# Kernel optimization log

Hardware: AMD Instinct MI355X
Metric: run time of the kernel (lower is better)

Reference implementation:

```python
import jax, jax.numpy as jnp
import numpy as np

BITS = 4
MAXQ = (1 << BITS) - 1  # 15
GROUPSIZE = 128
IN_F = 8192
OUT_F = 8192
PACK = 32 // BITS  # 8 values per int32


def setup_inputs() -> dict:
    key = jax.random.key(0)
    k_x, k_w, k_z, k_s, k_b = jax.random.split(key, 5)
    groups = IN_F // GROUPSIZE
    x = jax.random.normal(k_x, (4, 32, IN_F), dtype=jnp.float32)
    # bit-packed int32 weight / zeros (random bit patterns are valid quantized data)
    qweight = jax.random.randint(k_w, (IN_F // PACK, OUT_F), 0, 2**31 - 1, dtype=jnp.int32)
    qzeros = jax.random.randint(k_z, (groups, OUT_F // PACK), 0, 2**31 - 1, dtype=jnp.int32)
    scales = (jax.random.uniform(k_s, (groups, OUT_F), dtype=jnp.float32) * 0.01 + 1e-3)
    g_idx = (jnp.arange(IN_F, dtype=jnp.int32) // GROUPSIZE).astype(jnp.int32)
    bias = jax.random.normal(k_b, (OUT_F,), dtype=jnp.float32) * 0.01
    return {"x": x, "qweight": qweight, "qzeros": qzeros, "scales": scales,
            "g_idx": g_idx, "bias": bias}


def _dequant(qweight, qzeros, scales, g_idx):
    shifts = jnp.arange(0, 32, BITS, dtype=jnp.int32)  # [PACK]
    # unpack weights along the input dim: [in/PACK, PACK, out] -> [in, out]
    w = (qweight[:, None, :] >> shifts[None, :, None]) & MAXQ
    w = w.reshape(-1, qweight.shape[1])
    # unpack zeros along the output dim: [groups, out/PACK, PACK] -> [groups, out]
    # GPTQ stores (zero - 1), so add 1 back
    z = ((qzeros[:, :, None] >> shifts[None, None, :]) & MAXQ) + 1
    z = z.reshape(qzeros.shape[0], -1)
    # per-group dequant: W[i, o] = scales[g_idx[i], o] * (w[i, o] - z[g_idx[i], o])
    W = scales[g_idx] * (w.astype(scales.dtype) - z[g_idx].astype(scales.dtype))
    return W  # [in, out]


def reference(x, qweight, qzeros, scales, g_idx, bias):
    W = _dequant(qweight, qzeros, scales, g_idx)
    out = jnp.einsum('bsi,io->bso', x, W) + bias
    return out
```

## Files before the change

### kernel.cpp

```cpp
#include <hip/hip_runtime.h>
#include <hip/hip_bf16.h>
#include <stdint.h>


#define IN_F 8192
#define OUT_F 8192
#define MROWS 128
#define KSPLIT 8
#define KCHUNK 1024
#define BM 64

typedef short short8_t __attribute__((ext_vector_type(8)));
typedef float float4_t __attribute__((ext_vector_type(4)));
typedef float float16_t __attribute__((ext_vector_type(16)));

__global__ void reduce_out(const unsigned short* __restrict__ part,
                           const float* __restrict__ bias,
                           float* __restrict__ out) {
  const int i = (blockIdx.x * 256 + threadIdx.x) * 4;
  const int o = i & (OUT_F - 1);
  float4_t s = *(const float4_t*)(bias + o);
#pragma unroll
  for (int sl = 0; sl < KSPLIT; ++sl) {
    union { ushort2 u2[2]; unsigned short us[4]; } p;
    *(uint2*)&p = *(const uint2*)(part + (size_t)sl * MROWS * OUT_F + i);
    s.x += __uint_as_float((unsigned)p.us[0] << 16);
    s.y += __uint_as_float((unsigned)p.us[1] << 16);
    s.z += __uint_as_float((unsigned)p.us[2] << 16);
    s.w += __uint_as_float((unsigned)p.us[3] << 16);
  }
  *(float4_t*)(out + i) = s;
}

__global__ __launch_bounds__(1024, 4) void gptq_gemm(
    const float* __restrict__ x,
    const int* __restrict__ qweight,
    const int* __restrict__ qzeros,
    const float* __restrict__ scales,
    unsigned short* __restrict__ part)
{
  __shared__ unsigned short As[BM * KCHUNK];

  const int tid  = threadIdx.x;
  const int lane = tid & 63;
  const int l31  = lane & 31;
  const int half = lane >> 5;
  const int wv   = tid >> 6;

  const int bid = blockIdx.x;
  const int kb  = bid >> 5;
  const int mb  = (bid >> 4) & 1;
  const int nb  = bid & 15;

  const int kc0 = kb * KCHUNK;
  const int m0  = mb * BM;
  const int g0  = kc0 >> 7;
  const int kp_base = (kc0 >> 3) + half;
  const int goff = (wv & 3) * 2;

  const int col = nb * 512 + wv * 32 + l31;

  int   qw[3][8];
  float sc[3];
  int   zq[3];

  auto prefetch = [&](int i, int buf) {
    const int ge = (i + goff) & 7;
    const int kp = kp_base + ge * 16;
#pragma unroll
    for (int ks = 0; ks < 8; ++ks)
      qw[buf][ks] = qweight[(size_t)(kp + ks * 2) * OUT_F + col];
    const int gg_abs = g0 + ge;
    sc[buf] = scales[gg_abs * OUT_F + col];
    zq[buf] = qzeros[gg_abs * (OUT_F / 8) + (col >> 3)];
  };

  prefetch(0, 0);
  prefetch(1, 1);

  for (int rq = 0; rq < 4; ++rq) {
    const int rl = wv * 4 + rq;
    const float* grow = x + (size_t)(m0 + rl) * IN_F + kc0;
#pragma unroll
    for (int hf = 0; hf < 2; ++hf) {
      const int p = hf * 64 + lane;
      const int c = (p & 0x70) | ((p ^ (rl & 15)) & 15);
      float4_t a = *(const float4_t*)(grow + c * 8);
      float4_t b = *(const float4_t*)(grow + c * 8 + 4);
      union { short8_t v; __hip_bfloat162 h[4]; } u;
      u.h[0] = __float22bfloat162_rn(make_float2(a.x, a.y));
      u.h[1] = __float22bfloat162_rn(make_float2(a.z, a.w));
      u.h[2] = __float22bfloat162_rn(make_float2(b.x, b.y));
      u.h[3] = __float22bfloat162_rn(make_float2(b.z, b.w));
      *(short8_t*)(As + ((size_t)rl * 128 + p) * 8) = u.v;
    }
  }
  __syncthreads();

  float16_t acc[2];
#pragma unroll
  for (int mt = 0; mt < 2; ++mt)
#pragma unroll
    for (int r = 0; r < 16; ++r) acc[mt][r] = 0.f;

#pragma unroll
  for (int g = 0; g < 8; ++g) {
    const int cur = g % 3;
    const int ge  = (g + goff) & 7;

    if (g + 2 < 8) prefetch(g + 2, (g + 2) % 3);

    const int z = ((zq[cur] >> (4 * (col & 7))) & 15) + 1;
    const float zb = -sc[cur] * (float)z;
    const float s = sc[cur];

#pragma unroll
    for (int ks = 0; ks < 8; ++ks) {
      const int c = ge * 16 + ks * 2 + half;
      const int p = (c & 0x70) | ((c ^ (l31 & 15)) & 15);

      short8_t af[2];
#pragma unroll
      for (int mt = 0; mt < 2; ++mt)
        af[mt] = *(const short8_t*)(As + ((size_t)(mt * 32 + l31) * 128 + p) * 8);

      union { short8_t v; unsigned u[4]; } bw;
      const unsigned q  = (unsigned)qw[cur][ks];
      const unsigned qe = q & 0x0F0F0F0Fu;
      const unsigned qo = (q >> 4) & 0x0F0F0F0Fu;
#pragma unroll
      for (int jj = 0; jj < 4; ++jj) {
        const float f0 = fmaf(s, (float)((qe >> (8 * jj)) & 0xffu), zb);
        const float f1 = fmaf(s, (float)((qo >> (8 * jj)) & 0xffu), zb);
        bw.u[jj] = __builtin_amdgcn_perm(__float_as_uint(f1), __float_as_uint(f0),
                                         0x07060302u);
      }

#pragma unroll
      for (int mt = 0; mt < 2; ++mt)
        acc[mt] = __builtin_amdgcn_mfma_f32_32x32x16_bf16(af[mt], bw.v, acc[mt], 0, 0, 0);
    }
  }

  unsigned short* base = part + (size_t)kb * (MROWS * OUT_F);
#pragma unroll
  for (int mt = 0; mt < 2; ++mt)
#pragma unroll
    for (int r = 0; r < 16; ++r) {
      const int row = (r & 3) + 8 * (r >> 2) + 4 * half;
      __hip_bfloat16 h = __float2bfloat16(acc[mt][r]);
      base[(size_t)(m0 + mt * 32 + row) * OUT_F + col] = *(unsigned short*)&h;
    }
}

extern "C" void kernel_launch(void* const* d_in, const int* in_sizes, int n_in,
                              void* d_out, int out_size, void* d_ws, size_t ws_size,
                              hipStream_t stream) {
  const float* x        = (const float*)d_in[0];
  const int*   qweight  = (const int*)d_in[1];
  const int*   qzeros   = (const int*)d_in[2];
  const float* scales   = (const float*)d_in[3];
  const float* bias     = (const float*)d_in[5];
  float* out = (float*)d_out;

  unsigned short* part = (unsigned short*)d_ws;

  gptq_gemm<<<dim3(256), 1024, 0, stream>>>(x, qweight, qzeros, scales, part);
  reduce_out<<<dim3((MROWS * OUT_F) / (256 * 4)), 256, 0, stream>>>(part, bias, out);
}
```

Before: 111.8 us.

## Cover all 128 rows per block with 16-way split-K to reuse dequantized weights

Adds a GEMM variant in which each block covers all 128 rows of x over a 512-wide K chunk, with split-K raised from 8 to 16. Each block now feeds dequantized weights into four MFMA row tiles instead of two, so every packed weight is loaded and dequantized once rather than once per M-half. The cost is twice the bf16 partial-sum traffic, since the reduction kernel now writes and reads 16 slices. The register prefetch ring also drops from three buffers to two. The original path stays as a fallback when the workspace is too small for 16 slices.

```diff
diff --git a/kernel.cpp b/kernel.cpp
--- a/kernel.cpp
+++ b/kernel.cpp
@@ -6,14 +6,12 @@
 #define IN_F 8192
 #define OUT_F 8192
 #define MROWS 128
-#define KSPLIT 8
-#define KCHUNK 1024
-#define BM 64
 
 typedef short short8_t __attribute__((ext_vector_type(8)));
 typedef float float4_t __attribute__((ext_vector_type(4)));
 typedef float float16_t __attribute__((ext_vector_type(16)));
 
+template<int NSL>
 __global__ void reduce_out(const unsigned short* __restrict__ part,
                            const float* __restrict__ bias,
                            float* __restrict__ out) {
@@ -21,9 +19,9 @@
   const int o = i & (OUT_F - 1);
   float4_t s = *(const float4_t*)(bias + o);
 #pragma unroll
-  for (int sl = 0; sl < KSPLIT; ++sl) {
-    union { ushort2 u2[2]; unsigned short us[4]; } p;
-    *(uint2*)&p = *(const uint2*)(part + (size_t)sl * MROWS * OUT_F + i);
+  for (int sl = 0; sl < NSL; ++sl) {
+    union { uint2 u; unsigned short us[4]; } p;
+    p.u = *(const uint2*)(part + (size_t)sl * MROWS * OUT_F + i);
     s.x += __uint_as_float((unsigned)p.us[0] << 16);
     s.y += __uint_as_float((unsigned)p.us[1] << 16);
     s.z += __uint_as_float((unsigned)p.us[2] << 16);
@@ -32,14 +30,14 @@
   *(float4_t*)(out + i) = s;
 }
 
-__global__ __launch_bounds__(1024, 4) void gptq_gemm(
+__global__ __launch_bounds__(1024, 4) void gptq_gemm_bm128(
     const float* __restrict__ x,
     const int* __restrict__ qweight,
     const int* __restrict__ qzeros,
     const float* __restrict__ scales,
     unsigned short* __restrict__ part)
 {
-  __shared__ unsigned short As[BM * KCHUNK];
+  __shared__ unsigned short As[MROWS * 512];
 
   const int tid  = threadIdx.x;
   const int lane = tid & 63;
@@ -48,12 +46,127 @@
   const int wv   = tid >> 6;
 
   const int bid = blockIdx.x;
+  const int kb  = bid >> 4;
+  const int nb  = bid & 15;
+
+  const int kc0 = kb * 512;
+  const int g0  = kc0 >> 7;
+  const int kp_base = (kc0 >> 3) + half;
+  const int goff = wv & 3;
+
+  const int col = nb * 512 + wv * 32 + l31;
+
+  int   qw[2][8];
+  float sc[2];
+  int   zq[2];
+
+  auto prefetch = [&](int i, int buf) {
+    const int ge = (i + goff) & 3;
+    const int kp = kp_base + ge * 16;
+#pragma unroll
+    for (int ks = 0; ks < 8; ++ks)
+      qw[buf][ks] = qweight[(size_t)(kp + ks * 2) * OUT_F + col];
+    const int gg_abs = g0 + ge;
+    sc[buf] = scales[gg_abs * OUT_F + col];
+    zq[buf] = qzeros[gg_abs * (OUT_F / 8) + (col >> 3)];
+  };
+
+  prefetch(0, 0);
+
+  for (int rq = 0; rq < 8; ++rq) {
+    const int rl = wv * 8 + rq;
+    const float* grow = x + (size_t)rl * IN_F + kc0;
+    const int p = lane;
+    const int c = (p & ~15) | ((p ^ (rl & 15)) & 15);
+    float4_t a = *(const float4_t*)(grow + c * 8);
+    float4_t b = *(const float4_t*)(grow + c * 8 + 4);
+    union { short8_t v; __hip_bfloat162 h[4]; } u;
+    u.h[0] = __float22bfloat162_rn(make_float2(a.x, a.y));
+    u.h[1] = __float22bfloat162_rn(make_float2(a.z, a.w));
+    u.h[2] = __float22bfloat162_rn(make_float2(b.x, b.y));
+    u.h[3] = __float22bfloat162_rn(make_float2(b.z, b.w));
+    *(short8_t*)(As + ((size_t)rl * 64 + p) * 8) = u.v;
+  }
+  __syncthreads();
+
+  float16_t acc[4];
+#pragma unroll
+  for (int mt = 0; mt < 4; ++mt)
+#pragma unroll
+    for (int r = 0; r < 16; ++r) acc[mt][r] = 0.f;
+
+#pragma unroll
+  for (int g = 0; g < 4; ++g) {
+    const int cur = g & 1;
+    const int ge  = (g + goff) & 3;
+
+    if (g + 1 < 4) prefetch(g + 1, (g + 1) & 1);
+
+    const int z = ((zq[cur] >> (4 * (col & 7))) & 15) + 1;
+    const float zb = -sc[cur] * (float)z;
+    const float s = sc[cur];
+
+#pragma unroll
+    for (int ks = 0; ks < 8; ++ks) {
+      const int c = ge * 16 + ks * 2 + half;
+      const int p = (c & ~15) | ((c ^ (l31 & 15)) & 15);
+
+      short8_t af[4];
+#pragma unroll
+      for (int mt = 0; mt < 4; ++mt)
+        af[mt] = *(const short8_t*)(As + ((size_t)(mt * 32 + l31) * 64 + p) * 8);
+
+      union { short8_t v; unsigned u[4]; } bw;
+      const unsigned q  = (unsigned)qw[cur][ks];
+      const unsigned qe = q & 0x0F0F0F0Fu;
+      const unsigned qo = (q >> 4) & 0x0F0F0F0Fu;
+#pragma unroll
+      for (int jj = 0; jj < 4; ++jj) {
+        const float f0 = fmaf(s, (float)((qe >> (8 * jj)) & 0xffu), zb);
+        const float f1 = fmaf(s, (float)((qo >> (8 * jj)) & 0xffu), zb);
+        bw.u[jj] = __builtin_amdgcn_perm(__float_as_uint(f1), __float_as_uint(f0),
+                                         0x07060302u);
+      }
+
+#pragma unroll
+      for (int mt = 0; mt < 4; ++mt)
+        acc[mt] = __builtin_amdgcn_mfma_f32_32x32x16_bf16(af[mt], bw.v, acc[mt], 0, 0, 0);
+    }
+  }
+
+  unsigned short* base = part + (size_t)kb * (MROWS * OUT_F);
+#pragma unroll
+  for (int mt = 0; mt < 4; ++mt)
+#pragma unroll
+    for (int r = 0; r < 16; ++r) {
+      const int row = (r & 3) + 8 * (r >> 2) + 4 * half;
+      __hip_bfloat16 h = __float2bfloat16(acc[mt][r]);
+      base[(size_t)(mt * 32 + row) * OUT_F + col] = *(unsigned short*)&h;
+    }
+}
+
+__global__ __launch_bounds__(1024, 4) void gptq_gemm_ks8(
+    const float* __restrict__ x,
+    const int* __restrict__ qweight,
+    const int* __restrict__ qzeros,
+    const float* __restrict__ scales,
+    unsigned short* __restrict__ part)
+{
+  __shared__ unsigned short As[64 * 1024];
+
+  const int tid  = threadIdx.x;
+  const int lane = tid & 63;
+  const int l31  = lane & 31;
+  const int half = lane >> 5;
+  const int wv   = tid >> 6;
+
+  const int bid = blockIdx.x;
   const int kb  = bid >> 5;
   const int mb  = (bid >> 4) & 1;
   const int nb  = bid & 15;
 
-  const int kc0 = kb * KCHUNK;
-  const int m0  = mb * BM;
+  const int kc0 = kb * 1024;
+  const int m0  = mb * 64;
   const int g0  = kc0 >> 7;
   const int kp_base = (kc0 >> 3) + half;
   const int goff = (wv & 3) * 2;
@@ -165,6 +278,12 @@
 
   unsigned short* part = (unsigned short*)d_ws;
 
-  gptq_gemm<<<dim3(256), 1024, 0, stream>>>(x, qweight, qzeros, scales, part);
-  reduce_out<<<dim3((MROWS * OUT_F) / (256 * 4)), 256, 0, stream>>>(part, bias, out);
-}
+  const size_t need16 = (size_t)16 * MROWS * OUT_F * sizeof(unsigned short);
+  if (ws_size >= need16) {
+    gptq_gemm_bm128<<<dim3(256), 1024, 0, stream>>>(x, qweight, qzeros, scales, part);
+    reduce_out<16><<<dim3((MROWS * OUT_F) / (256 * 4)), 256, 0, stream>>>(part, bias, out);
+  } else {
+    gptq_gemm_ks8<<<dim3(256), 1024, 0, stream>>>(x, qweight, qzeros, scales, part);
+    reduce_out<8><<<dim3((MROWS * OUT_F) / (256 * 4)), 256, 0, stream>>>(part, bias, out);
+  }
+}
```

After: 111.0 us. No clear change (-0.7%).

## Fuse split-K reduction into GEMM with full-K blocks and double-buffered activations

Applied to the files above, without the earlier changes.

Replaces the global split-K partial-sum buffer and separate reduction kernel with a single kernel. Each block now covers the full K range for a 64x64 output tile, streaming activations in 512-wide chunks through double-buffered LDS. The four K-phase waves are reduced through shared memory before bias is added and fp32 is written. This removes the bf16 partial round-trip and the second launch. The cost is more x reloads across the 128 column blocks and a syncthreads per chunk.

```diff
diff --git a/kernel.cpp b/kernel.cpp
--- a/kernel.cpp
+++ b/kernel.cpp
@@ -5,110 +5,90 @@
 
 #define IN_F 8192
 #define OUT_F 8192
-#define MROWS 128
-#define KSPLIT 8
-#define KCHUNK 1024
-#define BM 64
 
 typedef short short8_t __attribute__((ext_vector_type(8)));
 typedef float float4_t __attribute__((ext_vector_type(4)));
 typedef float float16_t __attribute__((ext_vector_type(16)));
 
-__global__ void reduce_out(const unsigned short* __restrict__ part,
-                           const float* __restrict__ bias,
-                           float* __restrict__ out) {
-  const int i = (blockIdx.x * 256 + threadIdx.x) * 4;
-  const int o = i & (OUT_F - 1);
-  float4_t s = *(const float4_t*)(bias + o);
-#pragma unroll
-  for (int sl = 0; sl < KSPLIT; ++sl) {
-    union { ushort2 u2[2]; unsigned short us[4]; } p;
-    *(uint2*)&p = *(const uint2*)(part + (size_t)sl * MROWS * OUT_F + i);
-    s.x += __uint_as_float((unsigned)p.us[0] << 16);
-    s.y += __uint_as_float((unsigned)p.us[1] << 16);
-    s.z += __uint_as_float((unsigned)p.us[2] << 16);
-    s.w += __uint_as_float((unsigned)p.us[3] << 16);
-  }
-  *(float4_t*)(out + i) = s;
-}
-
-__global__ __launch_bounds__(1024, 4) void gptq_gemm(
+__global__ __launch_bounds__(1024, 4) void gptq_fused(
     const float* __restrict__ x,
     const int* __restrict__ qweight,
     const int* __restrict__ qzeros,
     const float* __restrict__ scales,
-    unsigned short* __restrict__ part)
+    const float* __restrict__ bias,
+    float* __restrict__ out)
 {
-  __shared__ unsigned short As[BM * KCHUNK];
+  __shared__ __align__(16) unsigned short As[2][64 * 512];
 
   const int tid  = threadIdx.x;
   const int lane = tid & 63;
   const int l31  = lane & 31;
   const int half = lane >> 5;
   const int wv   = tid >> 6;
+  const int ph   = wv & 3;
+  const int wc   = (wv >> 2) & 1;
+  const int wr   = wv >> 3;
 
   const int bid = blockIdx.x;
-  const int kb  = bid >> 5;
-  const int mb  = (bid >> 4) & 1;
-  const int nb  = bid & 15;
+  const int mb  = bid >> 7;
+  const int nb  = bid & 127;
+  const int m0  = mb * 64;
+  const int col = nb * 64 + wc * 32 + l31;
 
-  const int kc0 = kb * KCHUNK;
-  const int m0  = mb * BM;
-  const int g0  = kc0 >> 7;
-  const int kp_base = (kc0 >> 3) + half;
-  const int goff = (wv & 3) * 2;
+  const int kp_base = ph * 16 + half;
 
-  const int col = nb * 512 + wv * 32 + l31;
+  int   qw[2][8];
+  float sc[2];
+  int   zq[2];
 
-  int   qw[3][8];
-  float sc[3];
-  int   zq[3];
-
-  auto prefetch = [&](int i, int buf) {
-    const int ge = (i + goff) & 7;
-    const int kp = kp_base + ge * 16;
+  auto qpref = [&](int c, int buf) {
+    const int kp0 = c * 64 + kp_base;
 #pragma unroll
     for (int ks = 0; ks < 8; ++ks)
-      qw[buf][ks] = qweight[(size_t)(kp + ks * 2) * OUT_F + col];
-    const int gg_abs = g0 + ge;
-    sc[buf] = scales[gg_abs * OUT_F + col];
-    zq[buf] = qzeros[gg_abs * (OUT_F / 8) + (col >> 3)];
+      qw[buf][ks] = qweight[(size_t)(kp0 + ks * 2) * OUT_F + col];
+    const int gg = c * 4 + ph;
+    sc[buf] = scales[gg * OUT_F + col];
+    zq[buf] = qzeros[gg * (OUT_F / 8) + (col >> 3)];
   };
 
-  prefetch(0, 0);
-  prefetch(1, 1);
+  float4_t sa[4], sb[4];
+  auto stage_load = [&](int c) {
+#pragma unroll
+    for (int rq = 0; rq < 4; ++rq) {
+      const int rl = wv * 4 + rq;
+      const float* grow = x + (size_t)(m0 + rl) * IN_F + c * 512;
+      const int cc = (lane & ~15) | ((lane ^ (rl & 15)) & 15);
+      sa[rq] = *(const float4_t*)(grow + cc * 8);
+      sb[rq] = *(const float4_t*)(grow + cc * 8 + 4);
+    }
+  };
+  auto stage_write = [&](int b) {
+#pragma unroll
+    for (int rq = 0; rq < 4; ++rq) {
+      const int rl = wv * 4 + rq;
+      union { short8_t v; __hip_bfloat162 h[4]; } u;
+      u.h[0] = __float22bfloat162_rn(make_float2(sa[rq].x, sa[rq].y));
+      u.h[1] = __float22bfloat162_rn(make_float2(sa[rq].z, sa[rq].w));
+      u.h[2] = __float22bfloat162_rn(make_float2(sb[rq].x, sb[rq].y));
+      u.h[3] = __float22bfloat162_rn(make_float2(sb[rq].z, sb[rq].w));
+      *(short8_t*)(&As[b][((size_t)rl * 64 + lane) * 8]) = u.v;
+    }
+  };
 
-  for (int rq = 0; rq < 4; ++rq) {
-    const int rl = wv * 4 + rq;
-    const float* grow = x + (size_t)(m0 + rl) * IN_F + kc0;
-#pragma unroll
-    for (int hf = 0; hf < 2; ++hf) {
-      const int p = hf * 64 + lane;
-      const int c = (p & 0x70) | ((p ^ (rl & 15)) & 15);
-      float4_t a = *(const float4_t*)(grow + c * 8);
-      float4_t b = *(const float4_t*)(grow + c * 8 + 4);
-      union { short8_t v; __hip_bfloat162 h[4]; } u;
-      u.h[0] = __float22bfloat162_rn(make_float2(a.x, a.y));
-      u.h[1] = __float22bfloat162_rn(make_float2(a.z, a.w));
-      u.h[2] = __float22bfloat162_rn(make_float2(b.x, b.y));
-      u.h[3] = __float22bfloat162_rn(make_float2(b.z, b.w));
-      *(short8_t*)(As + ((size_t)rl * 128 + p) * 8) = u.v;
-    }
-  }
+  qpref(0, 0);
+  stage_load(0);
+  stage_write(0);
   __syncthreads();
 
-  float16_t acc[2];
+  float16_t acc;
 #pragma unroll
-  for (int mt = 0; mt < 2; ++mt)
-#pragma unroll
-    for (int r = 0; r < 16; ++r) acc[mt][r] = 0.f;
+  for (int r = 0; r < 16; ++r) acc[r] = 0.f;
 
-#pragma unroll
-  for (int g = 0; g < 8; ++g) {
-    const int cur = g % 3;
-    const int ge  = (g + goff) & 7;
+#pragma unroll 2
+  for (int c = 0; c < 16; ++c) {
+    const int cur = c & 1;
 
-    if (g + 2 < 8) prefetch(g + 2, (g + 2) % 3);
+    if (c + 1 < 16) { qpref(c + 1, cur ^ 1); stage_load(c + 1); }
 
     const int z = ((zq[cur] >> (4 * (col & 7))) & 15) + 1;
     const float zb = -sc[cur] * (float)z;
@@ -116,13 +96,10 @@
 
 #pragma unroll
     for (int ks = 0; ks < 8; ++ks) {
-      const int c = ge * 16 + ks * 2 + half;
-      const int p = (c & 0x70) | ((c ^ (l31 & 15)) & 15);
-
-      short8_t af[2];
-#pragma unroll
-      for (int mt = 0; mt < 2; ++mt)
-        af[mt] = *(const short8_t*)(As + ((size_t)(mt * 32 + l31) * 128 + p) * 8);
+      const int cL = ph * 16 + ks * 2 + half;
+      const int p  = (cL & ~15) | ((cL ^ (l31 & 15)) & 15);
+      const short8_t af =
+          *(const short8_t*)(&As[cur][((size_t)(wr * 32 + l31) * 64 + p) * 8]);
 
       union { short8_t v; unsigned u[4]; } bw;
       const unsigned q  = (unsigned)qw[cur][ks];
@@ -136,21 +113,44 @@
                                          0x07060302u);
       }
 
+      acc = __builtin_amdgcn_mfma_f32_32x32x16_bf16(af, bw.v, acc, 0, 0, 0);
+    }
+
+    if (c + 1 < 16) stage_write(cur ^ 1);
+    __syncthreads();
+  }
+
+  float* Ms = (float*)&As[0][0];
+  const int tile = wr * 2 + wc;
+  if (ph != 0) {
+    float* dst = Ms + (size_t)((tile * 3 + (ph - 1)) * 64 + lane) * 20;
 #pragma unroll
-      for (int mt = 0; mt < 2; ++mt)
-        acc[mt] = __builtin_amdgcn_mfma_f32_32x32x16_bf16(af[mt], bw.v, acc[mt], 0, 0, 0);
+    for (int q4 = 0; q4 < 4; ++q4) {
+      float4_t v;
+      v.x = acc[q4 * 4 + 0]; v.y = acc[q4 * 4 + 1];
+      v.z = acc[q4 * 4 + 2]; v.w = acc[q4 * 4 + 3];
+      *(float4_t*)(dst + q4 * 4) = v;
     }
   }
-
-  unsigned short* base = part + (size_t)kb * (MROWS * OUT_F);
+  __syncthreads();
+  if (ph == 0) {
 #pragma unroll
-  for (int mt = 0; mt < 2; ++mt)
+    for (int j = 0; j < 3; ++j) {
+      const float* src = Ms + (size_t)((tile * 3 + j) * 64 + lane) * 20;
+#pragma unroll
+      for (int q4 = 0; q4 < 4; ++q4) {
+        float4_t v = *(const float4_t*)(src + q4 * 4);
+        acc[q4 * 4 + 0] += v.x; acc[q4 * 4 + 1] += v.y;
+        acc[q4 * 4 + 2] += v.z; acc[q4 * 4 + 3] += v.w;
+      }
+    }
+    const float bcol = bias[col];
 #pragma unroll
     for (int r = 0; r < 16; ++r) {
       const int row = (r & 3) + 8 * (r >> 2) + 4 * half;
-      __hip_bfloat16 h = __float2bfloat16(acc[mt][r]);
-      base[(size_t)(m0 + mt * 32 + row) * OUT_F + col] = *(unsigned short*)&h;
+      out[(size_t)(m0 + wr * 32 + row) * OUT_F + col] = acc[r] + bcol;
     }
+  }
 }
 
 extern "C" void kernel_launch(void* const* d_in, const int* in_sizes, int n_in,
@@ -163,8 +163,7 @@
   const float* bias     = (const float*)d_in[5];
   float* out = (float*)d_out;
 
-  unsigned short* part = (unsigned short*)d_ws;
+  (void)d_ws; (void)ws_size;
 
-  gptq_gemm<<<dim3(256), 1024, 0, stream>>>(x, qweight, qzeros, scales, part);
-  reduce_out<<<dim3((MROWS * OUT_F) / (256 * 4)), 256, 0, stream>>>(part, bias, out);
+  gptq_fused<<<dim3(256), 1024, 0, stream>>>(x, qweight, qzeros, scales, bias, out);
 }
```

Result: slower. 123.2 us (+10.2%).
